# Optimization experiments

Hardware: AMD Instinct MI355X
Metric: run time of the kernel (lower is better)

Reference implementation:

```python
import jax, jax.numpy as jnp
import numpy as np

N_Q = 9      # qubits -> state dim 512
N_L = 10     # circuit layers
DIM = 2 ** N_Q
B = 16384    # batch
N_CLS = 10


def _apply_1q(psi, U, q):
    # psi: [B, 2,...,2] (N_Q qubit axes); U: [2,2] complex
    psi = jnp.moveaxis(psi, q + 1, 1)
    shp = psi.shape
    psi = jnp.einsum('ij,bjk->bik', U, psi.reshape(shp[0], 2, -1)).reshape(shp)
    return jnp.moveaxis(psi, 1, q + 1)


def _apply_2q(psi, U, q0, q1):
    # U: [4,4] complex acting on (q0, q1)
    psi = jnp.moveaxis(psi, (q0 + 1, q1 + 1), (1, 2))
    shp = psi.shape
    psi = jnp.einsum('ij,bjk->bik', U, psi.reshape(shp[0], 4, -1)).reshape(shp)
    return jnp.moveaxis(psi, (1, 2), (q0 + 1, q1 + 1))


def _rot_mat(phi, theta, omega):
    # PennyLane Rot = RZ(omega) RY(theta) RZ(phi)
    c, s = jnp.cos(theta / 2), jnp.sin(theta / 2)
    a, b = (phi + omega) / 2, (phi - omega) / 2
    return jnp.stack([
        jnp.stack([jnp.exp(-1j * a) * c, -jnp.exp(1j * b) * s]),
        jnp.stack([jnp.exp(-1j * b) * s, jnp.exp(1j * a) * c]),
    ]).astype(jnp.complex64)


def _crx_mat(t):
    c, s = jnp.cos(t / 2), jnp.sin(t / 2)
    rx = jnp.stack([jnp.stack([c + 0j, -1j * s]),
                    jnp.stack([-1j * s, c + 0j])]).astype(jnp.complex64)
    return jnp.eye(4, dtype=jnp.complex64).at[2:, 2:].set(rx)


def _layer(psi, rot_n, crx_n):
    for i in range(N_Q):
        psi = _apply_1q(psi, _rot_mat(rot_n[i, 0], rot_n[i, 1], rot_n[i, 2]), i)
    for i in range(N_Q):
        psi = _apply_2q(psi, _crx_mat(crx_n[i, 0]), i, (i + 1) % N_Q)
    return psi


def _circuit(x, rot, crx):
    # AmplitudeEmbedding(normalize=True)
    psi = (x / jnp.linalg.norm(x, axis=1, keepdims=True)).astype(jnp.complex64)
    psi = psi.reshape((x.shape[0],) + (2,) * N_Q)
    for n in range(N_L):
        psi = _layer(psi, rot[n], crx[n])
    probs = psi.real ** 2 + psi.imag ** 2
    # <Z_q> = P(bit_q = 0) - P(bit_q = 1)
    zs = []
    for q in range(N_Q):
        axes = tuple(a for a in range(1, N_Q + 1) if a != q + 1)
        p = probs.sum(axis=axes)  # [B, 2]
        zs.append(p[:, 0] - p[:, 1])
    return jnp.stack(zs, axis=1)  # [B, N_Q]


def setup_inputs() -> dict:
    key = jax.random.key(0)
    k0, k1, k2, k3, k4 = jax.random.split(key, 5)
    x = jax.random.normal(k0, (B, DIM), jnp.float32)
    rot = jax.random.normal(k1, (N_L, N_Q, 3), jnp.float32)
    crx = jax.random.normal(k2, (N_L, N_Q, 1), jnp.float32)
    fc_w = jax.random.normal(k3, (N_CLS, N_Q), jnp.float32) * 0.3
    fc_b = jax.random.normal(k4, (N_CLS,), jnp.float32) * 0.1
    return {"x": x, "rot": rot, "crx": crx, "fc_w": fc_w, "fc_b": fc_b}


def reference(x, rot, crx, fc_w, fc_b):
    z = _circuit(x, rot, crx)          # [B, 9]
    logits = z @ fc_w.T + fc_b         # [B, 10]
    return jax.nn.log_softmax(logits, axis=1)
```

## Files before the change

kernel.cpp:

```cpp
#include <hip/hip_runtime.h>
#include <hip/hip_bf16.h>
#include <math.h>

#define NQ 9
#define NL 10
#define DIM 512
#define NCLS 10
#define B_TOT 16384

#define A_OFF   ((size_t)0)
#define BT_OFF  ((size_t)16 << 20)
#define ZP_OFF  ((size_t)32 << 20)
#define GT_OFF  ((size_t)48 << 20)
#define WS_NEED (((size_t)96) << 20)

#if __has_builtin(__builtin_amdgcn_permlane16_swap) && __has_builtin(__builtin_amdgcn_permlane32_swap)
#define HAS_PL 1
#else
#define HAS_PL 0
#endif
typedef int iv2 __attribute__((ext_vector_type(2)));

__device__ __forceinline__ float shx(float v, int m) { return __shfl_xor(v, m, 64); }

template<int CTRL>
__device__ __forceinline__ float dppq(float v) {
  return __int_as_float(__builtin_amdgcn_update_dpp(
      0, __float_as_int(v), CTRL, 0xF, 0xF, true));
}

template<int M, bool PL>
__device__ __forceinline__ float shxt(float v) {
  if constexpr (M == 1)       return dppq<0xB1>(v);
  else if constexpr (M == 2)  return dppq<0x4E>(v);
  else if constexpr (M == 4)  return dppq<0x1B>(dppq<0x141>(v));
  else if constexpr (M == 8)  return dppq<0x128>(v);
  else if constexpr (M == 16) {
#if HAS_PL
    if constexpr (PL) {
      iv2 r = __builtin_amdgcn_permlane16_swap(__float_as_int(v), __float_as_int(v),
                                               false, false);
      return __int_as_float((threadIdx.x & 16) ? r.x : r.y);
    }
#endif
    return shx(v, 16);
  } else {
#if HAS_PL
    if constexpr (PL) {
      iv2 r = __builtin_amdgcn_permlane32_swap(__float_as_int(v), __float_as_int(v),
                                               false, false);
      return __int_as_float((threadIdx.x & 32) ? r.x : r.y);
    }
#endif
    return shx(v, 32);
  }
}

__device__ __forceinline__ int looks_bf16(const void* p, int count) {
  const unsigned short* u = (const unsigned short*)p;
  int n = count < 64 ? count : 64;
  int good = 0;
  for (int i = 0; i < n; ++i) {
    unsigned short v = u[i];
    int e = (v >> 7) & 0xFF;
    good += (e >= 100 && e <= 140) || ((v & 0x7FFF) == 0);
  }
  return good * 8 >= n * 7;
}

__device__ __forceinline__ float ld(const void* p, int i, int isbf) {
  if (isbf) return __uint_as_float(((unsigned)((const unsigned short*)p)[i]) << 16);
  return ((const float*)p)[i];
}

template<int M>
__device__ __forceinline__ void rot_x(float (&sr)[8], float (&si)[8], const float* u) {
  float4 uA = *(const float4*)u;
  float4 uB = *(const float4*)(u + 4);
  bool hi = (threadIdx.x & M) != 0;
  float ar = hi ? uB.z : uA.x, ai = hi ? uB.w : uA.y;
  float br = hi ? uB.x : uA.z, bi = hi ? uB.y : uA.w;
#pragma unroll
  for (int r = 0; r < 8; ++r) {
    float pr = shx(sr[r], M), pi = shx(si[r], M);
    float nr = ar * sr[r] - ai * si[r] + br * pr - bi * pi;
    float ni = ar * si[r] + ai * sr[r] + br * pi + bi * pr;
    sr[r] = nr; si[r] = ni;
  }
}
template<int S>
__device__ __forceinline__ void rot_r(float (&sr)[8], float (&si)[8], const float* u) {
  float4 uA = *(const float4*)u;
  float4 uB = *(const float4*)(u + 4);
#pragma unroll
  for (int r0 = 0; r0 < 8; ++r0) {
    if (r0 & S) continue;
    int r1 = r0 + S;
    float a0r = sr[r0], a0i = si[r0], a1r = sr[r1], a1i = si[r1];
    sr[r0] = uA.x * a0r - uA.y * a0i + uA.z * a1r - uA.w * a1i;
    si[r0] = uA.x * a0i + uA.y * a0r + uA.z * a1i + uA.w * a1r;
    sr[r1] = uB.x * a0r - uB.y * a0i + uB.z * a1r - uB.w * a1i;
    si[r1] = uB.x * a0i + uB.y * a0r + uB.z * a1i + uB.w * a1r;
  }
}
template<int MC, int MT>
__device__ __forceinline__ void crx_ll(float (&sr)[8], float (&si)[8], const float* cs) {
  bool ctrl = (threadIdx.x & MC) != 0;
  float c = ctrl ? cs[0] : 1.0f;
  float s = ctrl ? cs[1] : 0.0f;
#pragma unroll
  for (int r = 0; r < 8; ++r) {
    float pr = shx(sr[r], MT), pi = shx(si[r], MT);
    float nr = c * sr[r] + s * pi;
    float ni = c * si[r] - s * pr;
    sr[r] = nr; si[r] = ni;
  }
}
template<int MC, int ST>
__device__ __forceinline__ void crx_lr(float (&sr)[8], float (&si)[8], const float* cs) {
  bool ctrl = (threadIdx.x & MC) != 0;
  float c = ctrl ? cs[0] : 1.0f;
  float s = ctrl ? cs[1] : 0.0f;
#pragma unroll
  for (int r0 = 0; r0 < 8; ++r0) {
    if (r0 & ST) continue;
    int r1 = r0 + ST;
    float a0r = sr[r0], a0i = si[r0], a1r = sr[r1], a1i = si[r1];
    sr[r0] = c * a0r + s * a1i;  si[r0] = c * a0i - s * a1r;
    sr[r1] = c * a1r + s * a0i;  si[r1] = c * a1i - s * a0r;
  }
}
template<int PC, int ST>
__device__ __forceinline__ void crx_rr(float (&sr)[8], float (&si)[8], const float* cs) {
  float c = cs[0], s = cs[1];
#pragma unroll
  for (int r0 = 0; r0 < 8; ++r0) {
    if (r0 & ST) continue;
    if (!((r0 >> PC) & 1)) continue;
    int r1 = r0 + ST;
    float a0r = sr[r0], a0i = si[r0], a1r = sr[r1], a1i = si[r1];
    sr[r0] = c * a0r + s * a1i;  si[r0] = c * a0i - s * a1r;
    sr[r1] = c * a1r + s * a0i;  si[r1] = c * a1i - s * a0r;
  }
}
template<int PC, int MT>
__device__ __forceinline__ void crx_rl(float (&sr)[8], float (&si)[8], const float* cs) {
  float c = cs[0], s = cs[1];
#pragma unroll
  for (int r = 0; r < 8; ++r) {
    if (!((r >> PC) & 1)) continue;
    float pr = shx(sr[r], MT), pi = shx(si[r], MT);
    float nr = c * sr[r] + s * pi;
    float ni = c * si[r] - s * pr;
    sr[r] = nr; si[r] = ni;
  }
}

template<int M, bool PL>
__device__ __forceinline__ void rot_xb(float (&sr)[8], float (&si)[8], const float* u) {
  float4 uA = *(const float4*)u;
  float4 uB = *(const float4*)(u + 4);
  bool hi = (threadIdx.x & M) != 0;
  float ar = hi ? uB.z : uA.x, ai = hi ? uB.w : uA.y;
  float br = hi ? uB.x : uA.z, bi = hi ? uB.y : uA.w;
  float pr[8], pi[8];
#pragma unroll
  for (int r = 0; r < 8; ++r) { pr[r] = shxt<M, PL>(sr[r]); pi[r] = shxt<M, PL>(si[r]); }
#pragma unroll
  for (int r = 0; r < 8; ++r) {
    float nr = ar * sr[r] - ai * si[r] + br * pr[r] - bi * pi[r];
    float ni = ar * si[r] + ai * sr[r] + br * pi[r] + bi * pr[r];
    sr[r] = nr; si[r] = ni;
  }
}
template<int MC, int MT, bool PL>
__device__ __forceinline__ void crx_llb(float (&sr)[8], float (&si)[8], const float* cs) {
  bool ctrl = (threadIdx.x & MC) != 0;
  float c = ctrl ? cs[0] : 1.0f;
  float s = ctrl ? cs[1] : 0.0f;
  float pr[8], pi[8];
#pragma unroll
  for (int r = 0; r < 8; ++r) { pr[r] = shxt<MT, PL>(sr[r]); pi[r] = shxt<MT, PL>(si[r]); }
#pragma unroll
  for (int r = 0; r < 8; ++r) {
    float nr = c * sr[r] + s * pi[r];
    float ni = c * si[r] - s * pr[r];
    sr[r] = nr; si[r] = ni;
  }
}
template<bool PL>
__device__ __forceinline__ void crx_rlb032(float (&sr)[8], float (&si)[8], const float* cs) {
  float c = cs[0], s = cs[1];
  float pr[4], pi[4];
#pragma unroll
  for (int t = 0; t < 4; ++t) {
    int r = 2 * t + 1;
    pr[t] = shxt<32, PL>(sr[r]); pi[t] = shxt<32, PL>(si[r]);
  }
#pragma unroll
  for (int t = 0; t < 4; ++t) {
    int r = 2 * t + 1;
    float nr = c * sr[r] + s * pi[t];
    float ni = c * si[r] - s * pr[t];
    sr[r] = nr; si[r] = ni;
  }
}

__device__ __forceinline__ void build_gates(const void* rot, const void* crx,
                                            float* gU, float* gCS) {
  int tid = threadIdx.x;
  __shared__ int gflags[2];
  if (tid == 0) {
    gflags[0] = looks_bf16(rot, NL * NQ * 3);
    gflags[1] = looks_bf16(crx, NL * NQ);
  }
  __syncthreads();
  if (tid < NL * NQ) {
    int frot = gflags[0], fcrx = gflags[1];
    float phi = ld(rot, tid * 3 + 0, frot);
    float th  = ld(rot, tid * 3 + 1, frot);
    float om  = ld(rot, tid * 3 + 2, frot);
    float c = cosf(0.5f * th), s = sinf(0.5f * th);
    float a = 0.5f * (phi + om), b = 0.5f * (phi - om);
    float ca = cosf(a), sa = sinf(a), cb = cosf(b), sb = sinf(b);
    float* u = gU + tid * 8;
    u[0] =  ca * c; u[1] = -sa * c;
    u[2] = -cb * s; u[3] = -sb * s;
    u[4] =  cb * s; u[5] = -sb * s;
    u[6] =  ca * c; u[7] =  sa * c;
    float t2 = 0.5f * ld(crx, tid, fcrx);
    gCS[tid * 2 + 0] = cosf(t2);
    gCS[tid * 2 + 1] = sinf(t2);
  }
  __syncthreads();
}

__device__ __forceinline__ void run_circuit(float (&sr)[8], float (&si)[8],
                                            const float* gU, const float* gCS) {
#pragma unroll 1
  for (int n = 0; n < NL; ++n) {
    const float* U  = gU  + n * NQ * 8;
    const float* CS = gCS + n * NQ * 2;
    rot_x<32>(sr, si, U + 0 * 8);
    rot_x<16>(sr, si, U + 1 * 8);
    rot_x< 8>(sr, si, U + 2 * 8);
    rot_x< 4>(sr, si, U + 3 * 8);
    rot_x< 2>(sr, si, U + 4 * 8);
    rot_x< 1>(sr, si, U + 5 * 8);
    rot_r< 4>(sr, si, U + 6 * 8);
    rot_r< 2>(sr, si, U + 7 * 8);
    rot_r< 1>(sr, si, U + 8 * 8);
    crx_ll<32, 16>(sr, si, CS + 0 * 2);
    crx_ll<16,  8>(sr, si, CS + 1 * 2);
    crx_ll< 8,  4>(sr, si, CS + 2 * 2);
    crx_ll< 4,  2>(sr, si, CS + 3 * 2);
    crx_ll< 2,  1>(sr, si, CS + 4 * 2);
    crx_lr< 1,  4>(sr, si, CS + 5 * 2);
    crx_rr< 2,  2>(sr, si, CS + 6 * 2);
    crx_rr< 1,  1>(sr, si, CS + 7 * 2);
    crx_rl< 0, 32>(sr, si, CS + 8 * 2);
  }
}

template<bool PL>
__device__ __forceinline__ void run_circuit_v(float (&sr)[8], float (&si)[8],
                                              const float* __restrict__ gU,
                                              const float* __restrict__ gCS) {
#pragma unroll 1
  for (int n = 0; n < NL; ++n) {
    const float* U  = gU  + n * NQ * 8;
    const float* CS = gCS + n * NQ * 2;
    rot_xb<32, PL>(sr, si, U + 0 * 8);
    rot_xb<16, PL>(sr, si, U + 1 * 8);
    rot_xb< 8, PL>(sr, si, U + 2 * 8);
    rot_xb< 4, PL>(sr, si, U + 3 * 8);
    rot_xb< 2, PL>(sr, si, U + 4 * 8);
    rot_xb< 1, PL>(sr, si, U + 5 * 8);
    rot_r< 4>(sr, si, U + 6 * 8);
    rot_r< 2>(sr, si, U + 7 * 8);
    rot_r< 1>(sr, si, U + 8 * 8);
    crx_llb<32, 16, PL>(sr, si, CS + 0 * 2);
    crx_llb<16,  8, PL>(sr, si, CS + 1 * 2);
    crx_llb< 8,  4, PL>(sr, si, CS + 2 * 2);
    crx_llb< 4,  2, PL>(sr, si, CS + 3 * 2);
    crx_llb< 2,  1, PL>(sr, si, CS + 4 * 2);
    crx_lr< 1,  4>(sr, si, CS + 5 * 2);
    crx_rr< 2,  2>(sr, si, CS + 6 * 2);
    crx_rr< 1,  1>(sr, si, CS + 7 * 2);
    crx_rlb032<PL>(sr, si, CS + 8 * 2);
  }
}

__global__ __launch_bounds__(128) void gates_kernel(const void* __restrict__ rot,
                                                    const void* __restrict__ crx,
                                                    float* __restrict__ gG) {
  int tid = threadIdx.x;
  __shared__ int gflags[2];
  if (tid == 0) {
    gflags[0] = looks_bf16(rot, NL * NQ * 3);
    gflags[1] = looks_bf16(crx, NL * NQ);
  }
  __syncthreads();
  if (tid < NL * NQ) {
    int frot = gflags[0], fcrx = gflags[1];
    float phi = ld(rot, tid * 3 + 0, frot);
    float th  = ld(rot, tid * 3 + 1, frot);
    float om  = ld(rot, tid * 3 + 2, frot);
    float c = cosf(0.5f * th), s = sinf(0.5f * th);
    float a = 0.5f * (phi + om), b = 0.5f * (phi - om);
    float ca = cosf(a), sa = sinf(a), cb = cosf(b), sb = sinf(b);
    float* u = gG + tid * 8;
    u[0] =  ca * c; u[1] = -sa * c;
    u[2] = -cb * s; u[3] = -sb * s;
    u[4] =  cb * s; u[5] = -sb * s;
    u[6] =  ca * c; u[7] =  sa * c;
    float t2 = 0.5f * ld(crx, tid, fcrx);
    gG[720 + tid * 2 + 0] = cosf(t2);
    gG[720 + tid * 2 + 1] = sinf(t2);
  }
}

#define CIRC_BLKS 256
#define CAST_BLKS 2048

__global__ __launch_bounds__(128) void prep_kernel(const void* __restrict__ x,
                                                   const float* __restrict__ gG,
                                                   __hip_bfloat16* __restrict__ A,
                                                   __hip_bfloat16* __restrict__ BT) {
  int tid = threadIdx.x;
  if (blockIdx.x < CIRC_BLKS) {
    bool plok = false;
#if HAS_PL
    {
      int ln = tid & 63;
      iv2 r32 = __builtin_amdgcn_permlane32_swap(ln, ln, false, false);
      int p32 = (ln & 32) ? r32.x : r32.y;
      iv2 r16 = __builtin_amdgcn_permlane16_swap(ln, ln, false, false);
      int p16 = (ln & 16) ? r16.x : r16.y;
      plok = __all((p32 == (ln ^ 32)) && (p16 == (ln ^ 16))) != 0;
    }
#endif
    int lane = tid & 63, wv = tid >> 6;
    int k = blockIdx.x * 2 + wv;
    float sr[8], si[8];
#pragma unroll
    for (int r = 0; r < 8; ++r) {
      sr[r] = (lane * 8 + r == k) ? 1.f : 0.f;
      si[r] = 0.f;
    }
    if (plok) run_circuit_v<true>(sr, si, gG, gG + 720);
    else      run_circuit_v<false>(sr, si, gG, gG + 720);
#pragma unroll
    for (int r = 0; r < 8; ++r) {
      int j = lane * 8 + r;
      BT[(size_t)j * DIM + k]         = __float2bfloat16(sr[r]);
      BT[(size_t)(DIM + j) * DIM + k] = __float2bfloat16(si[r]);
    }
  } else {
    __shared__ int fx;
    if (tid == 0) fx = looks_bf16(x, B_TOT * DIM);
    __syncthreads();
    size_t stride = (size_t)CAST_BLKS * 128 * 8;
    for (size_t i0 = ((size_t)(blockIdx.x - CIRC_BLKS) * 128 + tid) * 8;
         i0 < (size_t)B_TOT * DIM; i0 += stride) {
      if (fx) {
        *(uint4*)(A + i0) = *(const uint4*)((const unsigned short*)x + i0);
      } else {
        const float4* src = (const float4*)((const float*)x + i0);
        float4 a = src[0], b = src[1];
        __hip_bfloat16 o[8];
        o[0] = __float2bfloat16(a.x); o[1] = __float2bfloat16(a.y);
        o[2] = __float2bfloat16(a.z); o[3] = __float2bfloat16(a.w);
        o[4] = __float2bfloat16(b.x); o[5] = __float2bfloat16(b.y);
        o[6] = __float2bfloat16(b.z); o[7] = __float2bfloat16(b.w);
        *(uint4*)(A + i0) = *(uint4*)o;
      }
    }
  }
}

using frag8 = __attribute__((ext_vector_type(8))) short;
using frag4 = __attribute__((ext_vector_type(4))) float;

typedef __attribute__((address_space(1))) const unsigned int GU32;
typedef __attribute__((address_space(3))) unsigned int LU32;
__device__ __forceinline__ void async16(const void* g, void* l) {
  __builtin_amdgcn_global_load_lds((GU32*)g, (LU32*)l, 16, 0, 0);
}

#define VM(N) asm volatile("s_waitcnt vmcnt(" #N ")" ::: "memory")
#define BARR  do { __builtin_amdgcn_sched_barrier(0); \
                   __builtin_amdgcn_s_barrier(); \
                   __builtin_amdgcn_sched_barrier(0); } while (0)

#define STG_A(NB, T1, H) do { \
  async16(gA + ((size_t)((H) * 128) * 512 + (T1) * 64),     dA + (NB) * 16384 + (H) * 8192); \
  async16(gA + ((size_t)((H) * 128 + 8) * 512 + (T1) * 64), dA + (NB) * 16384 + (H) * 8192 + 512); \
} while (0)
#define STG_B(NB, T1, H) do { \
  async16(gB + ((size_t)((H) * 128) * 512 + (T1) * 64),     dB + (NB) * 16384 + (H) * 8192); \
  async16(gB + ((size_t)((H) * 128 + 8) * 512 + (T1) * 64), dB + (NB) * 16384 + (H) * 8192 + 512); \
} while (0)

#define PHASE(CURB, QM, QN, STG, VMC) do { \
  frag8 paf[4][2], pbf[2][2]; \
  _Pragma("unroll") \
  for (int mi = 0; mi < 4; ++mi) { \
    _Pragma("unroll") \
    for (int kk = 0; kk < 2; ++kk) \
      paf[mi][kk] = *(const frag8*)(lsm + (CURB) * 16384 + \
        ((QM) * 128 + wm * 64 + mi * 16 + r15) * 64 + \
        (((kk * 4 + quad) ^ (r15 & 7)) * 8)); \
  } \
  _Pragma("unroll") \
  for (int ni = 0; ni < 2; ++ni) { \
    _Pragma("unroll") \
    for (int kk = 0; kk < 2; ++kk) \
      pbf[ni][kk] = *(const frag8*)(lsm + 32768 + (CURB) * 16384 + \
        ((QN) * 128 + wn * 32 + ni * 16 + r15) * 64 + \
        (((kk * 4 + quad) ^ (r15 & 7)) * 8)); \
  } \
  STG; \
  __builtin_amdgcn_s_setprio(1); \
  _Pragma("unroll") \
  for (int mi = 0; mi < 4; ++mi) { \
    _Pragma("unroll") \
    for (int ni = 0; ni < 2; ++ni) { \
      acc[QM][mi][QN][ni] = __builtin_amdgcn_mfma_f32_16x16x32_bf16( \
          paf[mi][0], pbf[ni][0], acc[QM][mi][QN][ni], 0, 0, 0); \
      acc[QM][mi][QN][ni] = __builtin_amdgcn_mfma_f32_16x16x32_bf16( \
          paf[mi][1], pbf[ni][1], acc[QM][mi][QN][ni], 0, 0, 0); \
    } \
  } \
  __builtin_amdgcn_s_setprio(0); \
  VMC; \
} while (0)

__global__ __launch_bounds__(512, 2) void gemm_z_kernel(const unsigned short* __restrict__ A,
                                                        const unsigned short* __restrict__ BT,
                                                        float* __restrict__ Zp) {
  __shared__ __align__(16) unsigned short lsm[65536];
  int bid = blockIdx.x;
  int xcd = bid & 7;
  int ii = bid >> 3;
  int m0 = (xcd * 8 + (ii >> 2)) * 256;
  int n0 = (ii & 3) * 256;
  int tid = threadIdx.x;
  int wv = tid >> 6, lane = tid & 63;
  int wm = wv >> 2, wn = wv & 3;
  int r15 = lane & 15, quad = lane >> 4;
  int lr3 = lane >> 3;
  int scol = ((lane & 7) ^ lr3) * 8;
  const unsigned short* gA = A + (size_t)(m0 + wv * 16 + lr3) * 512 + scol;
  const unsigned short* gB = BT + (size_t)(n0 + wv * 16 + lr3) * 512 + scol;
  unsigned short* dA = lsm + wv * 16 * 64;
  unsigned short* dB = lsm + 32768 + wv * 16 * 64;

  frag4 acc[2][4][2][2] = {};

  STG_A(0, 0, 0); STG_B(0, 0, 0); STG_A(0, 0, 1); STG_B(0, 0, 1);
  VM(4);
  BARR;

#pragma unroll 1
  for (int t = 0; t < 7; ++t) {
    const int cur = t & 1, nb = cur ^ 1;
    PHASE(cur, 0, 0, STG_A(nb, t + 1, 0), VM(4)); BARR;
    PHASE(cur, 1, 0, STG_B(nb, t + 1, 0), VM(4)); BARR;
    PHASE(cur, 0, 1, STG_A(nb, t + 1, 1), ;);
    PHASE(cur, 1, 1, STG_B(nb, t + 1, 1), VM(4)); BARR;
  }
  PHASE(1, 0, 0, ;, VM(2)); BARR;
  PHASE(1, 1, 0, ;, VM(0)); BARR;
  PHASE(1, 0, 1, ;, ;);
  PHASE(1, 1, 1, ;, ;);
  __syncthreads();

#pragma unroll
  for (int qm = 0; qm < 2; ++qm)
#pragma unroll
    for (int mi = 0; mi < 4; ++mi)
#pragma unroll
      for (int qn = 0; qn < 2; ++qn)
#pragma unroll
        for (int ni = 0; ni < 2; ++ni)
#pragma unroll
          for (int rg = 0; rg < 4; ++rg) {
            float v = acc[qm][mi][qn][ni][rg];
            float p = v * v;
            int prow = qm * 128 + wm * 64 + mi * 16 + quad * 4 + rg;
            int pcol = qn * 128 + wn * 32 + ni * 16 + r15;
            int phys = (pcol >> 3) ^ (prow & 7);
            __hip_bfloat16 h = __float2bfloat16(p);
            lsm[prow * 256 + phys * 8 + (pcol & 7)] = *(unsigned short*)&h;
          }
  __syncthreads();

  frag8 b2[8];
#pragma unroll
  for (int kk = 0; kk < 8; ++kk) {
    union { frag8 f; unsigned short u[8]; } bb;
#pragma unroll
    for (int e = 0; e < 8; ++e) {
      int j = (n0 + kk * 32 + quad * 8 + e) & 511;
      unsigned short us;
      if (r15 < 9)      us = ((((unsigned)j) >> ((8 - r15) & 31)) & 1) ? 0xBF80 : 0x3F80;
      else if (r15 == 9) us = 0x3F80;
      else               us = 0;
      bb.u[e] = us;
    }
    b2[kk] = bb.f;
  }
  frag4 z2[2] = {};
#pragma unroll
  for (int tt = 0; tt < 2; ++tt) {
    int mt = wv + tt * 8;
#pragma unroll
    for (int kk = 0; kk < 8; ++kk) {
      frag8 a2 = *(const frag8*)(lsm + (mt * 16 + r15) * 256 +
                                 (((kk * 4 + quad) ^ (r15 & 7)) * 8));
      z2[tt] = __builtin_amdgcn_mfma_f32_16x16x32_bf16(a2, b2[kk], z2[tt], 0, 0, 0);
    }
  }
  int panel = n0 >> 8;
  if (r15 < 10) {
#pragma unroll
    for (int tt = 0; tt < 2; ++tt) {
      int mt = wv + tt * 8;
#pragma unroll
      for (int rg = 0; rg < 4; ++rg) {
        int mrow = m0 + mt * 16 + quad * 4 + rg;
        Zp[(size_t)panel * (B_TOT * 10) + (size_t)mrow * 10 + r15] = z2[tt][rg];
      }
    }
  }
}

__global__ __launch_bounds__(128) void zred_kernel(const float* __restrict__ Zp,
                                                   const void* __restrict__ fcw,
                                                   const void* __restrict__ fcb,
                                                   float* __restrict__ out) {
  __shared__ int flags[2];
  __shared__ float sW[NCLS * NQ];
  __shared__ float sB[NCLS];
  int tid = threadIdx.x;
  if (tid == 0) {
    flags[0] = looks_bf16(fcw, NCLS * NQ);
    flags[1] = looks_bf16(fcb, NCLS);
  }
  __syncthreads();
  if (tid < NCLS * NQ) sW[tid] = ld(fcw, tid, flags[0]);
  if (tid < NCLS)      sB[tid] = ld(fcb, tid, flags[1]);
  __syncthreads();
  int row = blockIdx.x * 128 + tid;
  float z[10];
#pragma unroll
  for (int q = 0; q < 10; ++q) z[q] = 0.f;
#pragma unroll
  for (int pnl = 0; pnl < 4; ++pnl) {
    const float* p = Zp + (size_t)pnl * (B_TOT * 10) + (size_t)row * 10;
#pragma unroll
    for (int q = 0; q < 10; ++q) z[q] += p[q];
  }
  float invP = 1.0f / z[9];
#pragma unroll
  for (int q = 0; q < NQ; ++q) z[q] *= invP;
  float lg[NCLS], mx = -1e30f;
#pragma unroll
  for (int k = 0; k < NCLS; ++k) {
    float t = sB[k];
#pragma unroll
    for (int q = 0; q < NQ; ++q) t += z[q] * sW[k * NQ + q];
    lg[k] = t; mx = fmaxf(mx, t);
  }
  float se = 0.f;
#pragma unroll
  for (int k = 0; k < NCLS; ++k) se += expf(lg[k] - mx);
  float lse = mx + logf(se);
#pragma unroll
  for (int k = 0; k < NCLS; ++k) out[(size_t)row * NCLS + k] = lg[k] - lse;
}

__global__ __launch_bounds__(256) void qnn_kernel(
    const void* __restrict__ x, const void* __restrict__ rot,
    const void* __restrict__ crx, const void* __restrict__ fcw,
    const void* __restrict__ fcb, float* __restrict__ out) {
  __shared__ __align__(16) float gU[NL * NQ * 8];
  __shared__ __align__(16) float gCS[NL * NQ * 2];
  __shared__ int flags[3];
  int tid = threadIdx.x;
  if (tid == 0) {
    flags[0] = looks_bf16(x, B_TOT * DIM);
    flags[1] = looks_bf16(fcw, NCLS * NQ);
    flags[2] = looks_bf16(fcb, NCLS);
  }
  build_gates(rot, crx, gU, gCS);
  __syncthreads();
  int wid = (blockIdx.x * blockDim.x + tid) >> 6;
  int lane = tid & 63;
  float sr[8], si[8];
  if (flags[0]) {
    const uint4 u = *(const uint4*)((const unsigned short*)x + (size_t)wid * DIM + lane * 8);
    sr[0] = __uint_as_float(u.x << 16); sr[1] = __uint_as_float(u.x & 0xffff0000u);
    sr[2] = __uint_as_float(u.y << 16); sr[3] = __uint_as_float(u.y & 0xffff0000u);
    sr[4] = __uint_as_float(u.z << 16); sr[5] = __uint_as_float(u.z & 0xffff0000u);
    sr[6] = __uint_as_float(u.w << 16); sr[7] = __uint_as_float(u.w & 0xffff0000u);
  } else {
    const float4* xf = (const float4*)((const float*)x + (size_t)wid * DIM) + lane * 2;
    float4 a = xf[0], b = xf[1];
    sr[0] = a.x; sr[1] = a.y; sr[2] = a.z; sr[3] = a.w;
    sr[4] = b.x; sr[5] = b.y; sr[6] = b.z; sr[7] = b.w;
  }
  float nrm = 0.f;
#pragma unroll
  for (int r = 0; r < 8; ++r) { nrm += sr[r] * sr[r]; si[r] = 0.f; }
#pragma unroll
  for (int m = 1; m < 64; m <<= 1) nrm += shx(nrm, m);
  float inv = rsqrtf(nrm);
  inv = inv * (1.5f - 0.5f * nrm * inv * inv);
#pragma unroll
  for (int r = 0; r < 8; ++r) sr[r] *= inv;
  run_circuit(sr, si, gU, gCS);
  float p[8], P = 0.f;
#pragma unroll
  for (int r = 0; r < 8; ++r) { p[r] = sr[r] * sr[r] + si[r] * si[r]; P += p[r]; }
  float z[NQ];
#pragma unroll
  for (int q = 0; q < 6; ++q) z[q] = (lane & (32 >> q)) ? -P : P;
  z[6] = z[7] = z[8] = 0.f;
#pragma unroll
  for (int r = 0; r < 8; ++r) {
    z[6] += (r & 4) ? -p[r] : p[r];
    z[7] += (r & 2) ? -p[r] : p[r];
    z[8] += (r & 1) ? -p[r] : p[r];
  }
#pragma unroll
  for (int m = 1; m < 64; m <<= 1) {
#pragma unroll
    for (int q = 0; q < NQ; ++q) z[q] += shx(z[q], m);
  }
  int ffw = flags[1], ffb = flags[2];
  float lg[NCLS], mx = -1e30f;
#pragma unroll
  for (int k = 0; k < NCLS; ++k) {
    float t = ld(fcb, k, ffb);
#pragma unroll
    for (int q = 0; q < NQ; ++q) t += z[q] * ld(fcw, k * NQ + q, ffw);
    lg[k] = t; mx = fmaxf(mx, t);
  }
  float se = 0.f;
#pragma unroll
  for (int k = 0; k < NCLS; ++k) se += expf(lg[k] - mx);
  float lse = mx + logf(se);
  if (lane < NCLS) out[(size_t)wid * NCLS + lane] = lg[lane] - lse;
}

extern "C" void kernel_launch(void* const* d_in, const int* in_sizes, int n_in,
                              void* d_out, int out_size, void* d_ws, size_t ws_size,
                              hipStream_t stream) {
  const void* x   = d_in[0];
  const void* rot = d_in[1];
  const void* crx = d_in[2];
  const void* fcw = d_in[3];
  const void* fcb = d_in[4];
  float* out = (float*)d_out;
  if (ws_size >= WS_NEED) {
    __hip_bfloat16* A  = (__hip_bfloat16*)((char*)d_ws + A_OFF);
    __hip_bfloat16* BT = (__hip_bfloat16*)((char*)d_ws + BT_OFF);
    float*          Zp = (float*)((char*)d_ws + ZP_OFF);
    float*          gG = (float*)((char*)d_ws + GT_OFF);
    gates_kernel<<<1, 128, 0, stream>>>(rot, crx, gG);
    prep_kernel<<<CIRC_BLKS + CAST_BLKS, 128, 0, stream>>>(x, gG, A, BT);
    gemm_z_kernel<<<(B_TOT / 256) * (1024 / 256), 512, 0, stream>>>(
        (const unsigned short*)A, (const unsigned short*)BT, Zp);
    zred_kernel<<<B_TOT / 128, 128, 0, stream>>>(Zp, fcw, fcb, out);
  } else {
    qnn_kernel<<<(B_TOT * 64) / 256, 256, 0, stream>>>(x, rot, crx, fcw, fcb, out);
  }
}
```

Before: 155.6 us.

## Fuse gate construction into prep kernel and stage gates in shared memory

Removes the separate single-block gates_kernel launch. Each circuit block now builds the rotation and CRX coefficients itself into LDS, in a padded 20-float-per-layer layout. The per-layer gate loads become vectorized float4 LDS reads that are hoisted ahead of a sched_barrier. The aim is to cut one kernel launch plus its serialization gap, and to replace global gate reads with shared-memory reads, at the cost of every circuit block redundantly computing the trig values.

```diff
diff --git a/kernel.cpp b/kernel.cpp
--- a/kernel.cpp
+++ b/kernel.cpp
@@ -11,7 +11,6 @@
 #define A_OFF   ((size_t)0)
 #define BT_OFF  ((size_t)16 << 20)
 #define ZP_OFF  ((size_t)32 << 20)
-#define GT_OFF  ((size_t)48 << 20)
 #define WS_NEED (((size_t)96) << 20)
 
 #if __has_builtin(__builtin_amdgcn_permlane16_swap) && __has_builtin(__builtin_amdgcn_permlane32_swap)
@@ -157,9 +156,8 @@
 }
 
 template<int M, bool PL>
-__device__ __forceinline__ void rot_xb(float (&sr)[8], float (&si)[8], const float* u) {
-  float4 uA = *(const float4*)u;
-  float4 uB = *(const float4*)(u + 4);
+__device__ __forceinline__ void rot_xv(float (&sr)[8], float (&si)[8],
+                                       float4 uA, float4 uB) {
   bool hi = (threadIdx.x & M) != 0;
   float ar = hi ? uB.z : uA.x, ai = hi ? uB.w : uA.y;
   float br = hi ? uB.x : uA.z, bi = hi ? uB.y : uA.w;
@@ -173,11 +171,26 @@
     sr[r] = nr; si[r] = ni;
   }
 }
+template<int S>
+__device__ __forceinline__ void rot_rv(float (&sr)[8], float (&si)[8],
+                                       float4 uA, float4 uB) {
+#pragma unroll
+  for (int r0 = 0; r0 < 8; ++r0) {
+    if (r0 & S) continue;
+    int r1 = r0 + S;
+    float a0r = sr[r0], a0i = si[r0], a1r = sr[r1], a1i = si[r1];
+    sr[r0] = uA.x * a0r - uA.y * a0i + uA.z * a1r - uA.w * a1i;
+    si[r0] = uA.x * a0i + uA.y * a0r + uA.z * a1i + uA.w * a1r;
+    sr[r1] = uB.x * a0r - uB.y * a0i + uB.z * a1r - uB.w * a1i;
+    si[r1] = uB.x * a0i + uB.y * a0r + uB.z * a1i + uB.w * a1r;
+  }
+}
 template<int MC, int MT, bool PL>
-__device__ __forceinline__ void crx_llb(float (&sr)[8], float (&si)[8], const float* cs) {
+__device__ __forceinline__ void crx_llv(float (&sr)[8], float (&si)[8],
+                                        float cc, float ss) {
   bool ctrl = (threadIdx.x & MC) != 0;
-  float c = ctrl ? cs[0] : 1.0f;
-  float s = ctrl ? cs[1] : 0.0f;
+  float c = ctrl ? cc : 1.0f;
+  float s = ctrl ? ss : 0.0f;
   float pr[8], pi[8];
 #pragma unroll
   for (int r = 0; r < 8; ++r) { pr[r] = shxt<MT, PL>(sr[r]); pi[r] = shxt<MT, PL>(si[r]); }
@@ -188,9 +201,37 @@
     sr[r] = nr; si[r] = ni;
   }
 }
+template<int MC, int ST>
+__device__ __forceinline__ void crx_lrv(float (&sr)[8], float (&si)[8],
+                                        float cc, float ss) {
+  bool ctrl = (threadIdx.x & MC) != 0;
+  float c = ctrl ? cc : 1.0f;
+  float s = ctrl ? ss : 0.0f;
+#pragma unroll
+  for (int r0 = 0; r0 < 8; ++r0) {
+    if (r0 & ST) continue;
+    int r1 = r0 + ST;
+    float a0r = sr[r0], a0i = si[r0], a1r = sr[r1], a1i = si[r1];
+    sr[r0] = c * a0r + s * a1i;  si[r0] = c * a0i - s * a1r;
+    sr[r1] = c * a1r + s * a0i;  si[r1] = c * a1i - s * a0r;
+  }
+}
+template<int PC, int ST>
+__device__ __forceinline__ void crx_rrv(float (&sr)[8], float (&si)[8],
+                                        float c, float s) {
+#pragma unroll
+  for (int r0 = 0; r0 < 8; ++r0) {
+    if (r0 & ST) continue;
+    if (!((r0 >> PC) & 1)) continue;
+    int r1 = r0 + ST;
+    float a0r = sr[r0], a0i = si[r0], a1r = sr[r1], a1i = si[r1];
+    sr[r0] = c * a0r + s * a1i;  si[r0] = c * a0i - s * a1r;
+    sr[r1] = c * a1r + s * a0i;  si[r1] = c * a1i - s * a0r;
+  }
+}
 template<bool PL>
-__device__ __forceinline__ void crx_rlb032(float (&sr)[8], float (&si)[8], const float* cs) {
-  float c = cs[0], s = cs[1];
+__device__ __forceinline__ void crx_rlv032(float (&sr)[8], float (&si)[8],
+                                           float c, float s) {
   float pr[4], pi[4];
 #pragma unroll
   for (int t = 0; t < 4; ++t) {
@@ -263,60 +304,36 @@
 }
 
 template<bool PL>
-__device__ __forceinline__ void run_circuit_v(float (&sr)[8], float (&si)[8],
-                                              const float* __restrict__ gU,
-                                              const float* __restrict__ gCS) {
+__device__ __forceinline__ void run_circuit_L(float (&sr)[8], float (&si)[8],
+                                              const float* gU, const float* gC20) {
 #pragma unroll 1
   for (int n = 0; n < NL; ++n) {
-    const float* U  = gU  + n * NQ * 8;
-    const float* CS = gCS + n * NQ * 2;
-    rot_xb<32, PL>(sr, si, U + 0 * 8);
-    rot_xb<16, PL>(sr, si, U + 1 * 8);
-    rot_xb< 8, PL>(sr, si, U + 2 * 8);
-    rot_xb< 4, PL>(sr, si, U + 3 * 8);
-    rot_xb< 2, PL>(sr, si, U + 4 * 8);
-    rot_xb< 1, PL>(sr, si, U + 5 * 8);
-    rot_r< 4>(sr, si, U + 6 * 8);
-    rot_r< 2>(sr, si, U + 7 * 8);
-    rot_r< 1>(sr, si, U + 8 * 8);
-    crx_llb<32, 16, PL>(sr, si, CS + 0 * 2);
-    crx_llb<16,  8, PL>(sr, si, CS + 1 * 2);
-    crx_llb< 8,  4, PL>(sr, si, CS + 2 * 2);
-    crx_llb< 4,  2, PL>(sr, si, CS + 3 * 2);
-    crx_llb< 2,  1, PL>(sr, si, CS + 4 * 2);
-    crx_lr< 1,  4>(sr, si, CS + 5 * 2);
-    crx_rr< 2,  2>(sr, si, CS + 6 * 2);
-    crx_rr< 1,  1>(sr, si, CS + 7 * 2);
-    crx_rlb032<PL>(sr, si, CS + 8 * 2);
-  }
-}
-
-__global__ __launch_bounds__(128) void gates_kernel(const void* __restrict__ rot,
-                                                    const void* __restrict__ crx,
-                                                    float* __restrict__ gG) {
-  int tid = threadIdx.x;
-  __shared__ int gflags[2];
-  if (tid == 0) {
-    gflags[0] = looks_bf16(rot, NL * NQ * 3);
-    gflags[1] = looks_bf16(crx, NL * NQ);
-  }
-  __syncthreads();
-  if (tid < NL * NQ) {
-    int frot = gflags[0], fcrx = gflags[1];
-    float phi = ld(rot, tid * 3 + 0, frot);
-    float th  = ld(rot, tid * 3 + 1, frot);
-    float om  = ld(rot, tid * 3 + 2, frot);
-    float c = cosf(0.5f * th), s = sinf(0.5f * th);
-    float a = 0.5f * (phi + om), b = 0.5f * (phi - om);
-    float ca = cosf(a), sa = sinf(a), cb = cosf(b), sb = sinf(b);
-    float* u = gG + tid * 8;
-    u[0] =  ca * c; u[1] = -sa * c;
-    u[2] = -cb * s; u[3] = -sb * s;
-    u[4] =  cb * s; u[5] = -sb * s;
-    u[6] =  ca * c; u[7] =  sa * c;
-    float t2 = 0.5f * ld(crx, tid, fcrx);
-    gG[720 + tid * 2 + 0] = cosf(t2);
-    gG[720 + tid * 2 + 1] = sinf(t2);
+    const float4* Up = (const float4*)(gU + n * 72);
+    const float4* Cp = (const float4*)(gC20 + n * 20);
+    float4 u0 = Up[0],  u1 = Up[1],  u2 = Up[2],  u3 = Up[3],  u4 = Up[4];
+    float4 u5 = Up[5],  u6 = Up[6],  u7 = Up[7],  u8 = Up[8],  u9 = Up[9];
+    float4 u10 = Up[10], u11 = Up[11], u12 = Up[12], u13 = Up[13], u14 = Up[14];
+    float4 u15 = Up[15], u16 = Up[16], u17 = Up[17];
+    float4 c0 = Cp[0], c1 = Cp[1], c2 = Cp[2], c3 = Cp[3], c4 = Cp[4];
+    __builtin_amdgcn_sched_barrier(0);
+    rot_xv<32, PL>(sr, si, u0,  u1);
+    rot_xv<16, PL>(sr, si, u2,  u3);
+    rot_xv< 8, PL>(sr, si, u4,  u5);
+    rot_xv< 4, PL>(sr, si, u6,  u7);
+    rot_xv< 2, PL>(sr, si, u8,  u9);
+    rot_xv< 1, PL>(sr, si, u10, u11);
+    rot_rv< 4>(sr, si, u12, u13);
+    rot_rv< 2>(sr, si, u14, u15);
+    rot_rv< 1>(sr, si, u16, u17);
+    crx_llv<32, 16, PL>(sr, si, c0.x, c0.y);
+    crx_llv<16,  8, PL>(sr, si, c0.z, c0.w);
+    crx_llv< 8,  4, PL>(sr, si, c1.x, c1.y);
+    crx_llv< 4,  2, PL>(sr, si, c1.z, c1.w);
+    crx_llv< 2,  1, PL>(sr, si, c2.x, c2.y);
+    crx_lrv< 1,  4>(sr, si, c2.z, c2.w);
+    crx_rrv< 2,  2>(sr, si, c3.x, c3.y);
+    crx_rrv< 1,  1>(sr, si, c3.z, c3.w);
+    crx_rlv032<PL>(sr, si, c4.x, c4.y);
   }
 }
 
@@ -324,11 +341,42 @@
 #define CAST_BLKS 2048
 
 __global__ __launch_bounds__(128) void prep_kernel(const void* __restrict__ x,
-                                                   const float* __restrict__ gG,
+                                                   const void* __restrict__ rot,
+                                                   const void* __restrict__ crx,
                                                    __hip_bfloat16* __restrict__ A,
                                                    __hip_bfloat16* __restrict__ BT) {
   int tid = threadIdx.x;
   if (blockIdx.x < CIRC_BLKS) {
+    __shared__ __align__(16) float gU[NL * 72];
+    __shared__ __align__(16) float gC[NL * 20];
+    {
+      __shared__ int gflags[2];
+      if (tid == 0) {
+        gflags[0] = looks_bf16(rot, NL * NQ * 3);
+        gflags[1] = looks_bf16(crx, NL * NQ);
+      }
+      __syncthreads();
+      if (tid < NL * NQ) {
+        int frot = gflags[0], fcrx = gflags[1];
+        float phi = ld(rot, tid * 3 + 0, frot);
+        float th  = ld(rot, tid * 3 + 1, frot);
+        float om  = ld(rot, tid * 3 + 2, frot);
+        float c = cosf(0.5f * th), s = sinf(0.5f * th);
+        float a = 0.5f * (phi + om), b = 0.5f * (phi - om);
+        float ca = cosf(a), sa = sinf(a), cb = cosf(b), sb = sinf(b);
+        float* u = gU + tid * 8;
+        u[0] =  ca * c; u[1] = -sa * c;
+        u[2] = -cb * s; u[3] = -sb * s;
+        u[4] =  cb * s; u[5] = -sb * s;
+        u[6] =  ca * c; u[7] =  sa * c;
+        int n = tid / 9, q = tid - n * 9;
+        float t2 = 0.5f * ld(crx, tid, fcrx);
+        gC[n * 20 + q * 2 + 0] = cosf(t2);
+        gC[n * 20 + q * 2 + 1] = sinf(t2);
+      }
+      if (tid < NL * 2) gC[(tid >> 1) * 20 + 18 + (tid & 1)] = 0.f;
+      __syncthreads();
+    }
     bool plok = false;
 #if HAS_PL
     {
@@ -348,8 +396,8 @@
       sr[r] = (lane * 8 + r == k) ? 1.f : 0.f;
       si[r] = 0.f;
     }
-    if (plok) run_circuit_v<true>(sr, si, gG, gG + 720);
-    else      run_circuit_v<false>(sr, si, gG, gG + 720);
+    if (plok) run_circuit_L<true>(sr, si, gU, gC);
+    else      run_circuit_L<false>(sr, si, gU, gC);
 #pragma unroll
     for (int r = 0; r < 8; ++r) {
       int j = lane * 8 + r;
@@ -668,9 +716,7 @@
     __hip_bfloat16* A  = (__hip_bfloat16*)((char*)d_ws + A_OFF);
     __hip_bfloat16* BT = (__hip_bfloat16*)((char*)d_ws + BT_OFF);
     float*          Zp = (float*)((char*)d_ws + ZP_OFF);
-    float*          gG = (float*)((char*)d_ws + GT_OFF);
-    gates_kernel<<<1, 128, 0, stream>>>(rot, crx, gG);
-    prep_kernel<<<CIRC_BLKS + CAST_BLKS, 128, 0, stream>>>(x, gG, A, BT);
+    prep_kernel<<<CIRC_BLKS + CAST_BLKS, 128, 0, stream>>>(x, rot, crx, A, BT);
     gemm_z_kernel<<<(B_TOT / 256) * (1024 / 256), 512, 0, stream>>>(
         (const unsigned short*)A, (const unsigned short*)BT, Zp);
     zred_kernel<<<B_TOT / 128, 128, 0, stream>>>(Zp, fcw, fcb, out);
```

New measurement: 139.7 us. -10.2%, faster.
